# Optimization experiments

Hardware: AMD Instinct MI355X
Metric: run time of the kernel (lower is better)

## Reference

```python
import jax, jax.numpy as jnp
import numpy as np

HEADS = 4
DIM_HEAD = 128


def setup_inputs() -> dict:
    key = jax.random.key(0)
    k1, k2, k3 = jax.random.split(key, 3)
    dim = 256
    hidden = HEADS * DIM_HEAD  # 512
    x = jax.random.normal(k1, (16, dim, 64, 64), dtype=jnp.float32)
    # 1x1 conv weights stored as [out_ch, in_ch] (kernel dims squeezed)
    w_qkv = jax.random.normal(k2, (hidden * 3, dim), dtype=jnp.float32) * (1.0 / np.sqrt(dim))
    w_out = jax.random.normal(k3, (dim, hidden), dtype=jnp.float32) * (1.0 / np.sqrt(hidden))
    b_out = jnp.zeros((dim,), dtype=jnp.float32)
    return {"x": x, "w_qkv": w_qkv, "w_out": w_out, "b_out": b_out}


def reference(x, w_qkv, w_out, b_out):
    b, c, h, w = x.shape
    n = h * w
    # 1x1 conv == per-pixel linear projection
    qkv = jnp.einsum('bchw,oc->bohw', x, w_qkv)           # [b, 3*heads*dh, h, w]
    qkv = qkv.reshape(b, 3, HEADS, DIM_HEAD, n)           # 'b (qkv heads c) h w -> qkv b heads c (h w)'
    q, k, v = qkv[:, 0], qkv[:, 1], qkv[:, 2]             # [b, heads, dh, n]
    k = jax.nn.softmax(k, axis=-1)                        # softmax over spatial positions
    context = jnp.einsum('bhdn,bhen->bhde', k, v)         # [b, heads, dh, dh]
    out = jnp.einsum('bhde,bhdn->bhen', context, q)       # [b, heads, dh, n]
    out = out.reshape(b, HEADS * DIM_HEAD, h, w)          # 'b heads c (h w) -> b (heads c) h w'
    y = jnp.einsum('bchw,oc->bohw', out, w_out) + b_out[None, :, None, None]
    return y
```

## Files before the change

kernel.cpp:

```cpp
#include <hip/hip_runtime.h>

#define BATCH 16
#define CIN   256
#define NSP   4096
#define HID   512

typedef short v8s __attribute__((ext_vector_type(8)));
typedef float v4f __attribute__((ext_vector_type(4)));

__device__ __forceinline__ unsigned short f2bf(float f) {
    union { float f; unsigned u; } a; a.f = f;
    unsigned r = a.u + 0x7fffu + ((a.u >> 16) & 1u);
    return (unsigned short)(r >> 16);
}
__device__ __forceinline__ float bf2f(unsigned short s) {
    union { unsigned u; float f; } a; a.u = ((unsigned)s) << 16;
    return a.f;
}

__device__ __forceinline__ void gld_lds16(const unsigned short* g, unsigned short* l) {
    __builtin_amdgcn_global_load_lds(
        (const __attribute__((address_space(1))) unsigned int*)g,
        (__attribute__((address_space(3))) unsigned int*)l,
        16, 0, 0);
}

__global__ __launch_bounds__(256) void k_cvt_w(const float* __restrict__ wq,
                                               unsigned short* __restrict__ wbf) {
    const int t = blockIdx.x * 256 + threadIdx.x;
    const float4 f0 = *(const float4*)(wq + (size_t)t * 8);
    const float4 f1 = *(const float4*)(wq + (size_t)t * 8 + 4);
    union { unsigned short s[8]; uint4 u; } p;
    p.s[0] = f2bf(f0.x); p.s[1] = f2bf(f0.y); p.s[2] = f2bf(f0.z); p.s[3] = f2bf(f0.w);
    p.s[4] = f2bf(f1.x); p.s[5] = f2bf(f1.y); p.s[6] = f2bf(f1.z); p.s[7] = f2bf(f1.w);
    *(uint4*)(wbf + (size_t)t * 8) = p.u;
}

__global__ __launch_bounds__(256) void k_tr_wq(const float* __restrict__ wq,
                                               unsigned short* __restrict__ wqT) {
    __shared__ float tile[64 * 65];
    const int t = threadIdx.x;
    const int u0 = blockIdx.x * 64, c0 = blockIdx.y * 64;
    {
        const int cl = (t & 15) * 4, ul = t >> 4;
        #pragma unroll
        for (int i = 0; i < 4; i++) {
            int u = ul + i * 16;
            const float4 f = *(const float4*)(wq + (size_t)(u0 + u) * CIN + c0 + cl);
            *(float4*)(&tile[u * 65 + cl]) = f;
        }
    }
    __syncthreads();
    {
        const int ul4 = (t & 15) * 4, cl = t >> 4;
        #pragma unroll
        for (int i = 0; i < 4; i++) {
            int c = cl + i * 16;
            union { unsigned short s[4]; uint2 u; } p;
            #pragma unroll
            for (int j = 0; j < 4; j++)
                p.s[j] = f2bf(tile[(ul4 + j) * 65 + c]);
            *(uint2*)(wqT + (size_t)(c0 + c) * HID + u0 + ul4) = p.u;
        }
    }
}

__global__ __launch_bounds__(256) void k_prep(const float* __restrict__ x,
                                              unsigned short* __restrict__ xbf,
                                              unsigned short* __restrict__ xT) {
    __shared__ float tile[64 * 65];
    const int t = threadIdx.x;
    const int n0 = blockIdx.x * 64, c0 = blockIdx.y * 64, bz = blockIdx.z;
    const float* xb = x + (size_t)bz * CIN * NSP;
    {
        const int nl = (t & 15) * 4, cl = t >> 4;
        #pragma unroll
        for (int i = 0; i < 4; i++) {
            int c = cl + i * 16;
            const float4 f = *(const float4*)(xb + (size_t)(c0 + c) * NSP + n0 + nl);
            *(float4*)(&tile[c * 65 + nl]) = f;
            union { unsigned short s[4]; uint2 u; } p;
            p.s[0] = f2bf(f.x); p.s[1] = f2bf(f.y); p.s[2] = f2bf(f.z); p.s[3] = f2bf(f.w);
            *(uint2*)(xbf + ((size_t)bz * CIN + c0 + c) * NSP + n0 + nl) = p.u;
        }
    }
    __syncthreads();
    {
        const int cl4 = (t & 15) * 4, nl = t >> 4;
        #pragma unroll
        for (int i = 0; i < 4; i++) {
            int n = nl + i * 16;
            union { unsigned short s[4]; uint2 u; } p;
            #pragma unroll
            for (int j = 0; j < 4; j++)
                p.s[j] = f2bf(tile[(cl4 + j) * 65 + n]);
            *(uint2*)(xT + ((size_t)bz * NSP + n0 + n) * CIN + c0 + cl4) = p.u;
        }
    }
}

__global__ __launch_bounds__(256) void k_k(const unsigned short* __restrict__ wbf,
                                           const unsigned short* __restrict__ xT,
                                           unsigned short* __restrict__ expk,
                                           float* __restrict__ zp) {
    __shared__ __align__(16) unsigned short As[128 * 32];
    __shared__ __align__(16) unsigned short Bs[128 * 32];
    const int t = threadIdx.x;
    const int id = blockIdx.x;
    const int bz = id >> 7;
    const int r  = id & 127;
    const int xcd = r & 7, s = r >> 3;
    const int bn = (xcd << 2) | (s & 3);
    const int bm = s >> 2;
    const int m0 = bm * 128, n0 = bn * 128;
    const int lane = t & 63, wv = t >> 6;
    const int quad = lane >> 4, l15 = lane & 15;
    const int wm = (wv & 1) * 64, wn = (wv >> 1) * 64;

    const int srow = lane >> 2, scol = (lane & 3) * 8;
    unsigned short* Al0 = As + wv * 16 * 32;
    unsigned short* Al1 = Al0 + 64 * 32;
    unsigned short* Bl0 = Bs + wv * 16 * 32;
    unsigned short* Bl1 = Bl0 + 64 * 32;
    const unsigned short* Ag0 = wbf + (size_t)(512 + m0 + wv * 16 + srow) * CIN + scol;
    const unsigned short* Ag1 = Ag0 + 64 * CIN;
    const unsigned short* Bg0 = xT + ((size_t)bz * NSP + n0 + wv * 16 + srow) * CIN + scol;
    const unsigned short* Bg1 = Bg0 + 64 * CIN;

    v4f acc[4][4];
    #pragma unroll
    for (int i = 0; i < 4; i++)
        #pragma unroll
        for (int j = 0; j < 4; j++) acc[i][j] = (v4f)0.f;

    for (int kk = 0; kk < CIN; kk += 32) {
        gld_lds16(Ag0 + kk, Al0);
        gld_lds16(Ag1 + kk, Al1);
        gld_lds16(Bg0 + kk, Bl0);
        gld_lds16(Bg1 + kk, Bl1);
        __syncthreads();
        v8s af[4], bfr[4];
        #pragma unroll
        for (int mi = 0; mi < 4; mi++) {
            union { v8s v; uint4 u; } rr;
            rr.u = *(const uint4*)(&As[(wm + mi * 16 + l15) * 32 + quad * 8]);
            af[mi] = rr.v;
        }
        #pragma unroll
        for (int ni = 0; ni < 4; ni++) {
            union { v8s v; uint4 u; } rr;
            rr.u = *(const uint4*)(&Bs[(wn + ni * 16 + l15) * 32 + quad * 8]);
            bfr[ni] = rr.v;
        }
        #pragma unroll
        for (int mi = 0; mi < 4; mi++)
            #pragma unroll
            for (int ni = 0; ni < 4; ni++)
                acc[mi][ni] = __builtin_amdgcn_mfma_f32_16x16x32_bf16(af[mi], bfr[ni], acc[mi][ni], 0, 0, 0);
        __syncthreads();
    }

    float zr[4][4];
    #pragma unroll
    for (int mi = 0; mi < 4; mi++)
        #pragma unroll
        for (int rr = 0; rr < 4; rr++) zr[mi][rr] = 0.f;
    #pragma unroll
    for (int mi = 0; mi < 4; mi++)
        #pragma unroll
        for (int ni = 0; ni < 4; ni++)
            #pragma unroll
            for (int rr = 0; rr < 4; rr++) {
                float e = __expf(acc[mi][ni][rr]);
                acc[mi][ni][rr] = e;
                zr[mi][rr] += e;
            }
    #pragma unroll
    for (int mi = 0; mi < 4; mi++) {
        int row = m0 + wm + mi * 16 + quad * 4;
        #pragma unroll
        for (int ni = 0; ni < 4; ni++) {
            int n = n0 + wn + ni * 16 + l15;
            #pragma unroll
            for (int rr = 0; rr < 4; rr++)
                expk[((size_t)bz * 512 + row + rr) * NSP + n] = f2bf(acc[mi][ni][rr]);
        }
    }
    const int half = wv >> 1;
    #pragma unroll
    for (int mi = 0; mi < 4; mi++)
        #pragma unroll
        for (int rr = 0; rr < 4; rr++) {
            float z = zr[mi][rr];
            z += __shfl_xor(z, 1); z += __shfl_xor(z, 2);
            z += __shfl_xor(z, 4); z += __shfl_xor(z, 8);
            if (l15 == 0)
                zp[((size_t)bz * 512 + m0 + wm + mi * 16 + quad * 4 + rr) * 64 + bn * 2 + half] = z;
        }
}

__global__ __launch_bounds__(256) void k_S(const unsigned short* __restrict__ expk,
                                           const unsigned short* __restrict__ xbf,
                                           float* __restrict__ Sp) {
    __shared__ __align__(16) unsigned short As[128 * 32];
    __shared__ __align__(16) unsigned short Bs[128 * 32];
    const int t = threadIdx.x;
    const int id = blockIdx.x;
    const int hc = id >> 6;
    const int h = hc >> 1, ch = hc & 1;
    const int bkc = id & 63;
    const int b = bkc >> 2, kc = bkc & 3;
    const int kw = kc * 1024;
    const int lane = t & 63, wv = t >> 6, quad = lane >> 4, l15 = lane & 15;
    const int wm = (wv & 1) * 64, wn = (wv >> 1) * 64;

    const int srow = lane >> 2, scol = (lane & 3) * 8;
    unsigned short* Al0 = As + wv * 16 * 32;
    unsigned short* Al1 = Al0 + 64 * 32;
    unsigned short* Bl0 = Bs + wv * 16 * 32;
    unsigned short* Bl1 = Bl0 + 64 * 32;
    const unsigned short* Ag0 = expk + ((size_t)b * 512 + h * 128 + wv * 16 + srow) * NSP + kw + scol;
    const unsigned short* Ag1 = Ag0 + 64 * NSP;
    const unsigned short* Bg0 = xbf + ((size_t)b * CIN + ch * 128 + wv * 16 + srow) * NSP + kw + scol;
    const unsigned short* Bg1 = Bg0 + 64 * NSP;

    v4f acc[4][4];
    #pragma unroll
    for (int i = 0; i < 4; i++)
        #pragma unroll
        for (int j = 0; j < 4; j++) acc[i][j] = (v4f)0.f;

    for (int kk = 0; kk < 1024; kk += 32) {
        gld_lds16(Ag0 + kk, Al0);
        gld_lds16(Ag1 + kk, Al1);
        gld_lds16(Bg0 + kk, Bl0);
        gld_lds16(Bg1 + kk, Bl1);
        __syncthreads();
        v8s af[4], bfr[4];
        #pragma unroll
        for (int mi = 0; mi < 4; mi++) {
            union { v8s v; uint4 u; } rr;
            rr.u = *(const uint4*)(&As[(wm + mi * 16 + l15) * 32 + quad * 8]);
            af[mi] = rr.v;
        }
        #pragma unroll
        for (int ni = 0; ni < 4; ni++) {
            union { v8s v; uint4 u; } rr;
            rr.u = *(const uint4*)(&Bs[(wn + ni * 16 + l15) * 32 + quad * 8]);
            bfr[ni] = rr.v;
        }
        #pragma unroll
        for (int mi = 0; mi < 4; mi++)
            #pragma unroll
            for (int ni = 0; ni < 4; ni++)
                acc[mi][ni] = __builtin_amdgcn_mfma_f32_16x16x32_bf16(af[mi], bfr[ni], acc[mi][ni], 0, 0, 0);
        __syncthreads();
    }

    const int bh = b * 4 + h;
    float* outp = Sp + ((size_t)(bh * 2 + ch) * 4 + kc) * 16384;
    #pragma unroll
    for (int mi = 0; mi < 4; mi++)
        #pragma unroll
        for (int ni = 0; ni < 4; ni++)
            #pragma unroll
            for (int rr = 0; rr < 4; rr++)
                outp[(wm + mi * 16 + quad * 4 + rr) * 128 + wn + ni * 16 + l15] = acc[mi][ni][rr];
}

__global__ __launch_bounds__(256) void k_sred(const float* __restrict__ Sp,
                                              unsigned short* __restrict__ Sred) {
    const int qv = blockIdx.x * 256 + threadIdx.x;
    const int bh = qv >> 13, r = qv & 8191;
    const int dl = r >> 6, cq6 = r & 63;
    const int ch = cq6 >> 5, clq = cq6 & 31;
    const float* p = Sp + ((size_t)(bh * 2 + ch) * 4) * 16384 + dl * 128 + clq * 4;
    float4 s = *(const float4*)p;
    #pragma unroll
    for (int kc = 1; kc < 4; kc++) {
        const float4 f = *(const float4*)(p + (size_t)kc * 16384);
        s.x += f.x; s.y += f.y; s.z += f.z; s.w += f.w;
    }
    union { unsigned short us[4]; uint2 u; } pk;
    pk.us[0] = f2bf(s.x); pk.us[1] = f2bf(s.y); pk.us[2] = f2bf(s.z); pk.us[3] = f2bf(s.w);
    *(uint2*)(Sred + (size_t)bh * 32768 + dl * 256 + cq6 * 4) = pk.u;
}

__global__ __launch_bounds__(256) void k_redwc(const unsigned short* __restrict__ Sred,
                                               const float* __restrict__ zp,
                                               const unsigned short* __restrict__ wbf,
                                               const float* __restrict__ w_out,
                                               unsigned short* __restrict__ Wc) {
    __shared__ unsigned short Ds[128 * 136];
    __shared__ float zinv[128];
    const int t = threadIdx.x;
    const int bh = blockIdx.x;  const int b = bh >> 2, h = bh & 3;
    const int lane = t & 63, wv = t >> 6, quad = lane >> 4, l15 = lane & 15;

    if (t < 128) {
        float z = 0.f;
        #pragma unroll
        for (int nt = 0; nt < 64; nt++)
            z += zp[((size_t)b * 512 + h * 128 + t) * 64 + nt];
        zinv[t] = 1.0f / z;
    }
    __syncthreads();

    {
        const int wm = (wv & 1) * 64, wn = (wv >> 1) * 64;
        const unsigned short* Sb = Sred + (size_t)bh * 32768;
        const unsigned short* Vb = wbf + (size_t)(1024 + h * 128) * CIN;
        v4f acc[4][4];
        #pragma unroll
        for (int i = 0; i < 4; i++)
            #pragma unroll
            for (int j = 0; j < 4; j++) acc[i][j] = (v4f)0.f;
        for (int kk = 0; kk < CIN; kk += 32) {
            v8s af[4], bfr[4];
            #pragma unroll
            for (int mi = 0; mi < 4; mi++) {
                union { v8s v; uint4 u; } rr;
                rr.u = *(const uint4*)(Sb + (size_t)(wm + mi * 16 + l15) * 256 + kk + quad * 8);
                af[mi] = rr.v;
            }
            #pragma unroll
            for (int ni = 0; ni < 4; ni++) {
                union { v8s v; uint4 u; } rr;
                rr.u = *(const uint4*)(Vb + (size_t)(wn + ni * 16 + l15) * 256 + kk + quad * 8);
                bfr[ni] = rr.v;
            }
            #pragma unroll
            for (int mi = 0; mi < 4; mi++)
                #pragma unroll
                for (int ni = 0; ni < 4; ni++)
                    acc[mi][ni] = __builtin_amdgcn_mfma_f32_16x16x32_bf16(af[mi], bfr[ni], acc[mi][ni], 0, 0, 0);
        }
        float zq[4][4];
        #pragma unroll
        for (int mi = 0; mi < 4; mi++)
            #pragma unroll
            for (int rr = 0; rr < 4; rr++)
                zq[mi][rr] = zinv[wm + mi * 16 + quad * 4 + rr];
        #pragma unroll
        for (int mi = 0; mi < 4; mi++)
            #pragma unroll
            for (int ni = 0; ni < 4; ni++)
                #pragma unroll
                for (int rr = 0; rr < 4; rr++)
                    Ds[(wm + mi * 16 + quad * 4 + rr) * 136 + wn + ni * 16 + l15] =
                        f2bf(acc[mi][ni][rr] * zq[mi][rr]);
    }
    __syncthreads();

    {
        const int wm = wv * 64;
        v4f acc[4][8];
        #pragma unroll
        for (int i = 0; i < 4; i++)
            #pragma unroll
            for (int j = 0; j < 8; j++) acc[i][j] = (v4f)0.f;
        for (int kk = 0; kk < 128; kk += 32) {
            v8s af[4], bfr[8];
            #pragma unroll
            for (int mi = 0; mi < 4; mi++) {
                int o = wm + mi * 16 + l15;
                const float* wp = w_out + (size_t)o * HID + h * 128 + kk + quad * 8;
                float4 f0 = *(const float4*)wp;
                float4 f1 = *(const float4*)(wp + 4);
                union { v8s v; unsigned short s[8]; } r;
                r.s[0] = f2bf(f0.x); r.s[1] = f2bf(f0.y); r.s[2] = f2bf(f0.z); r.s[3] = f2bf(f0.w);
                r.s[4] = f2bf(f1.x); r.s[5] = f2bf(f1.y); r.s[6] = f2bf(f1.z); r.s[7] = f2bf(f1.w);
                af[mi] = r.v;
            }
            #pragma unroll
            for (int ni = 0; ni < 8; ni++) {
                const unsigned short* p = &Ds[(ni * 16 + l15) * 136 + kk + quad * 8];
                union { v8s v; uint4 u; } r;
                r.u = *(const uint4*)p;
                bfr[ni] = r.v;
            }
            #pragma unroll
            for (int mi = 0; mi < 4; mi++)
                #pragma unroll
                for (int ni = 0; ni < 8; ni++)
                    acc[mi][ni] = __builtin_amdgcn_mfma_f32_16x16x32_bf16(af[mi], bfr[ni], acc[mi][ni], 0, 0, 0);
        }
        #pragma unroll
        for (int ni = 0; ni < 8; ni++) {
            int d = ni * 16 + l15;
            #pragma unroll
            for (int mi = 0; mi < 4; mi++)
                #pragma unroll
                for (int rr = 0; rr < 4; rr++) {
                    int o = wm + mi * 16 + quad * 4 + rr;
                    Wc[((size_t)b * 256 + o) * HID + h * 128 + d] = f2bf(acc[mi][ni][rr]);
                }
        }
    }
}

__global__ __launch_bounds__(256) void k_chain(const unsigned short* __restrict__ Wc,
                                               const unsigned short* __restrict__ wqT,
                                               unsigned short* __restrict__ Weff) {
    __shared__ __align__(16) unsigned short As[128 * 32];
    __shared__ __align__(16) unsigned short Bs[128 * 32];
    const int t = threadIdx.x;
    const int m0 = blockIdx.x * 128, n0 = blockIdx.y * 128, bz = blockIdx.z;
    const int lane = t & 63, wv = t >> 6, quad = lane >> 4, l15 = lane & 15;
    const int wm = (wv & 1) * 64, wn = (wv >> 1) * 64;

    const int srow = lane >> 2, scol = (lane & 3) * 8;
    unsigned short* Al0 = As + wv * 16 * 32;
    unsigned short* Al1 = Al0 + 64 * 32;
    unsigned short* Bl0 = Bs + wv * 16 * 32;
    unsigned short* Bl1 = Bl0 + 64 * 32;
    const unsigned short* Ag0 = Wc + ((size_t)bz * 256 + m0 + wv * 16 + srow) * HID + scol;
    const unsigned short* Ag1 = Ag0 + 64 * HID;
    const unsigned short* Bg0 = wqT + (size_t)(n0 + wv * 16 + srow) * HID + scol;
    const unsigned short* Bg1 = Bg0 + 64 * HID;

    v4f acc[4][4];
    #pragma unroll
    for (int i = 0; i < 4; i++)
        #pragma unroll
        for (int j = 0; j < 4; j++) acc[i][j] = (v4f)0.f;

    for (int kk = 0; kk < HID; kk += 32) {
        gld_lds16(Ag0 + kk, Al0);
        gld_lds16(Ag1 + kk, Al1);
        gld_lds16(Bg0 + kk, Bl0);
        gld_lds16(Bg1 + kk, Bl1);
        __syncthreads();
        v8s af[4], bfr[4];
        #pragma unroll
        for (int mi = 0; mi < 4; mi++) {
            union { v8s v; uint4 u; } rr;
            rr.u = *(const uint4*)(&As[(wm + mi * 16 + l15) * 32 + quad * 8]);
            af[mi] = rr.v;
        }
        #pragma unroll
        for (int ni = 0; ni < 4; ni++) {
            union { v8s v; uint4 u; } rr;
            rr.u = *(const uint4*)(&Bs[(wn + ni * 16 + l15) * 32 + quad * 8]);
            bfr[ni] = rr.v;
        }
        #pragma unroll
        for (int mi = 0; mi < 4; mi++)
            #pragma unroll
            for (int ni = 0; ni < 4; ni++)
                acc[mi][ni] = __builtin_amdgcn_mfma_f32_16x16x32_bf16(af[mi], bfr[ni], acc[mi][ni], 0, 0, 0);
        __syncthreads();
    }
    #pragma unroll
    for (int mi = 0; mi < 4; mi++) {
        int obase = m0 + wm + mi * 16 + quad * 4;
        #pragma unroll
        for (int ni = 0; ni < 4; ni++) {
            int c = n0 + wn + ni * 16 + l15;
            #pragma unroll
            for (int r = 0; r < 4; r++)
                Weff[((size_t)bz * 256 + obase + r) * 256 + c] = f2bf(acc[mi][ni][r]);
        }
    }
}

__global__ __launch_bounds__(256) void k_y(const unsigned short* __restrict__ Weff,
                                           const unsigned short* __restrict__ xT,
                                           const float* __restrict__ b_out,
                                           float* __restrict__ y) {
    __shared__ __align__(16) unsigned short As[128 * 32];
    __shared__ __align__(16) unsigned short Bs[128 * 32];
    const int t = threadIdx.x;
    const int m0 = blockIdx.x * 128;
    const int n0 = blockIdx.y * 128;
    const int bz = blockIdx.z;
    const int lane = t & 63, wv = t >> 6, quad = lane >> 4, l15 = lane & 15;
    const int wm = (wv & 1) * 64, wn = (wv >> 1) * 64;

    const int srow = lane >> 2, scol = (lane & 3) * 8;
    unsigned short* Al0 = As + wv * 16 * 32;
    unsigned short* Al1 = Al0 + 64 * 32;
    unsigned short* Bl0 = Bs + wv * 16 * 32;
    unsigned short* Bl1 = Bl0 + 64 * 32;
    const unsigned short* Ag0 = Weff + ((size_t)bz * 256 + m0 + wv * 16 + srow) * CIN + scol;
    const unsigned short* Ag1 = Ag0 + 64 * CIN;
    const unsigned short* Bg0 = xT + ((size_t)bz * NSP + n0 + wv * 16 + srow) * CIN + scol;
    const unsigned short* Bg1 = Bg0 + 64 * CIN;

    v4f acc[4][4];
    #pragma unroll
    for (int i = 0; i < 4; i++)
        #pragma unroll
        for (int j = 0; j < 4; j++) acc[i][j] = (v4f)0.f;

    for (int kk = 0; kk < CIN; kk += 32) {
        gld_lds16(Ag0 + kk, Al0);
        gld_lds16(Ag1 + kk, Al1);
        gld_lds16(Bg0 + kk, Bl0);
        gld_lds16(Bg1 + kk, Bl1);
        __syncthreads();
        v8s af[4], bfr[4];
        #pragma unroll
        for (int mi = 0; mi < 4; mi++) {
            union { v8s v; uint4 u; } rr;
            rr.u = *(const uint4*)(&As[(wm + mi * 16 + l15) * 32 + quad * 8]);
            af[mi] = rr.v;
        }
        #pragma unroll
        for (int ni = 0; ni < 4; ni++) {
            union { v8s v; uint4 u; } rr;
            rr.u = *(const uint4*)(&Bs[(wn + ni * 16 + l15) * 32 + quad * 8]);
            bfr[ni] = rr.v;
        }
        #pragma unroll
        for (int mi = 0; mi < 4; mi++)
            #pragma unroll
            for (int ni = 0; ni < 4; ni++)
                acc[mi][ni] = __builtin_amdgcn_mfma_f32_16x16x32_bf16(af[mi], bfr[ni], acc[mi][ni], 0, 0, 0);
        __syncthreads();
    }
    #pragma unroll
    for (int mi = 0; mi < 4; mi++) {
        int o = m0 + wm + mi * 16 + quad * 4;
        #pragma unroll
        for (int ni = 0; ni < 4; ni++) {
            int n = n0 + wn + ni * 16 + l15;
            #pragma unroll
            for (int r = 0; r < 4; r++)
                y[((size_t)bz * 256 + o + r) * NSP + n] = acc[mi][ni][r] + b_out[o + r];
        }
    }
}

extern "C" void kernel_launch(void* const* d_in, const int* in_sizes, int n_in,
                              void* d_out, int out_size, void* d_ws, size_t ws_size,
                              hipStream_t stream) {
    (void)in_sizes; (void)n_in; (void)out_size; (void)ws_size;
    const float* x     = (const float*)d_in[0];
    const float* w_qkv = (const float*)d_in[1];
    const float* w_out = (const float*)d_in[2];
    const float* b_out = (const float*)d_in[3];
    float* y = (float*)d_out;
    char* ws = (char*)d_ws;

    unsigned short* xT   = (unsigned short*)(ws);
    unsigned short* xbf  = (unsigned short*)(ws + 33554432);
    unsigned short* expk = (unsigned short*)(ws + 67108864);
    float*          Sp   = (float*)(ws + 134217728);
    float*          zp   = (float*)(ws + 167772160);
    unsigned short* Sred = (unsigned short*)(ws + 176160768);
    unsigned short* Wc   = (unsigned short*)(ws + 180355072);
    unsigned short* Weff = (unsigned short*)(ws + 184549376);
    unsigned short* wbf  = (unsigned short*)(ws + 186646528);
    unsigned short* wqT  = (unsigned short*)(ws + 187432960);

    k_cvt_w<<<dim3(192),        256, 0, stream>>>(w_qkv, wbf);
    k_tr_wq<<<dim3(8, 4),       256, 0, stream>>>(w_qkv, wqT);
    k_prep <<<dim3(64, 4, 16),  256, 0, stream>>>(x, xbf, xT);
    k_k    <<<dim3(2048),       256, 0, stream>>>(wbf, xT, expk, zp);
    k_S    <<<dim3(512),        256, 0, stream>>>(expk, xbf, Sp);
    k_sred <<<dim3(2048),       256, 0, stream>>>(Sp, Sred);
    k_redwc<<<dim3(64),         256, 0, stream>>>(Sred, zp, wbf, w_out, Wc);
    k_chain<<<dim3(2, 2, 16),   256, 0, stream>>>(Wc, wqT, Weff);
    k_y    <<<dim3(2, 32, 16),  256, 0, stream>>>(Weff, xT, b_out, y);
}
```

Before: 262.2 us.

## Swap GEMM operand roles for vectorized epilogue stores and merge weight prep kernels

Swaps the A/B operands in the k_k, k_S, k_chain and k_y GEMMs so that each thread's four accumulator rows are contiguous along the output's fastest dimension. Epilogue stores become 8- or 16-byte vector writes instead of scalar 2- or 4-byte strided writes. The exp-sum reduction in k_k is redone to match the new fragment mapping. It also merges the two weight-preparation kernels into one launch to save a kernel launch. Store coalescing per instruction changes: lanes now spread across rows rather than along one row.

```diff
diff --git a/kernel.cpp b/kernel.cpp
--- a/kernel.cpp
+++ b/kernel.cpp
@@ -25,22 +25,24 @@
         16, 0, 0);
 }
 
-__global__ __launch_bounds__(256) void k_cvt_w(const float* __restrict__ wq,
-                                               unsigned short* __restrict__ wbf) {
-    const int t = blockIdx.x * 256 + threadIdx.x;
-    const float4 f0 = *(const float4*)(wq + (size_t)t * 8);
-    const float4 f1 = *(const float4*)(wq + (size_t)t * 8 + 4);
-    union { unsigned short s[8]; uint4 u; } p;
-    p.s[0] = f2bf(f0.x); p.s[1] = f2bf(f0.y); p.s[2] = f2bf(f0.z); p.s[3] = f2bf(f0.w);
-    p.s[4] = f2bf(f1.x); p.s[5] = f2bf(f1.y); p.s[6] = f2bf(f1.z); p.s[7] = f2bf(f1.w);
-    *(uint4*)(wbf + (size_t)t * 8) = p.u;
-}
-
-__global__ __launch_bounds__(256) void k_tr_wq(const float* __restrict__ wq,
-                                               unsigned short* __restrict__ wqT) {
+__global__ __launch_bounds__(256) void k_w(const float* __restrict__ wq,
+                                           unsigned short* __restrict__ wbf,
+                                           unsigned short* __restrict__ wqT) {
+    const int bid = blockIdx.x;
+    if (bid < 192) {
+        const int t = bid * 256 + threadIdx.x;
+        const float4 f0 = *(const float4*)(wq + (size_t)t * 8);
+        const float4 f1 = *(const float4*)(wq + (size_t)t * 8 + 4);
+        union { unsigned short s[8]; uint4 u; } p;
+        p.s[0] = f2bf(f0.x); p.s[1] = f2bf(f0.y); p.s[2] = f2bf(f0.z); p.s[3] = f2bf(f0.w);
+        p.s[4] = f2bf(f1.x); p.s[5] = f2bf(f1.y); p.s[6] = f2bf(f1.z); p.s[7] = f2bf(f1.w);
+        *(uint4*)(wbf + (size_t)t * 8) = p.u;
+        return;
+    }
     __shared__ float tile[64 * 65];
-    const int t = threadIdx.x;
-    const int u0 = blockIdx.x * 64, c0 = blockIdx.y * 64;
+    const int bb = bid - 192;
+    const int u0 = (bb & 7) * 64, c0 = (bb >> 3) * 64;
+    const int t = threadIdx.x;
     {
         const int cl = (t & 15) * 4, ul = t >> 4;
         #pragma unroll
@@ -112,19 +114,19 @@
     const int xcd = r & 7, s = r >> 3;
     const int bn = (xcd << 2) | (s & 3);
     const int bm = s >> 2;
-    const int m0 = bm * 128, n0 = bn * 128;
+    const int d0 = bm * 128, n0 = bn * 128;
     const int lane = t & 63, wv = t >> 6;
     const int quad = lane >> 4, l15 = lane & 15;
-    const int wm = (wv & 1) * 64, wn = (wv >> 1) * 64;
+    const int wmN = (wv & 1) * 64, wnD = (wv >> 1) * 64;
 
     const int srow = lane >> 2, scol = (lane & 3) * 8;
     unsigned short* Al0 = As + wv * 16 * 32;
     unsigned short* Al1 = Al0 + 64 * 32;
     unsigned short* Bl0 = Bs + wv * 16 * 32;
     unsigned short* Bl1 = Bl0 + 64 * 32;
-    const unsigned short* Ag0 = wbf + (size_t)(512 + m0 + wv * 16 + srow) * CIN + scol;
+    const unsigned short* Ag0 = xT + ((size_t)bz * NSP + n0 + wv * 16 + srow) * CIN + scol;
     const unsigned short* Ag1 = Ag0 + 64 * CIN;
-    const unsigned short* Bg0 = xT + ((size_t)bz * NSP + n0 + wv * 16 + srow) * CIN + scol;
+    const unsigned short* Bg0 = wbf + (size_t)(512 + d0 + wv * 16 + srow) * CIN + scol;
     const unsigned short* Bg1 = Bg0 + 64 * CIN;
 
     v4f acc[4][4];
@@ -143,13 +145,13 @@
         #pragma unroll
         for (int mi = 0; mi < 4; mi++) {
             union { v8s v; uint4 u; } rr;
-            rr.u = *(const uint4*)(&As[(wm + mi * 16 + l15) * 32 + quad * 8]);
+            rr.u = *(const uint4*)(&As[(wmN + mi * 16 + l15) * 32 + quad * 8]);
             af[mi] = rr.v;
         }
         #pragma unroll
         for (int ni = 0; ni < 4; ni++) {
             union { v8s v; uint4 u; } rr;
-            rr.u = *(const uint4*)(&Bs[(wn + ni * 16 + l15) * 32 + quad * 8]);
+            rr.u = *(const uint4*)(&Bs[(wnD + ni * 16 + l15) * 32 + quad * 8]);
             bfr[ni] = rr.v;
         }
         #pragma unroll
@@ -160,43 +162,31 @@
         __syncthreads();
     }
 
-    float zr[4][4];
-    #pragma unroll
-    for (int mi = 0; mi < 4; mi++)
-        #pragma unroll
-        for (int rr = 0; rr < 4; rr++) zr[mi][rr] = 0.f;
-    #pragma unroll
-    for (int mi = 0; mi < 4; mi++)
-        #pragma unroll
-        for (int ni = 0; ni < 4; ni++)
+    float zacc[4] = {0.f, 0.f, 0.f, 0.f};
+    #pragma unroll
+    for (int ni = 0; ni < 4; ni++) {
+        const int d = d0 + wnD + ni * 16 + l15;
+        #pragma unroll
+        for (int mi = 0; mi < 4; mi++) {
+            const int nb = n0 + wmN + mi * 16 + quad * 4;
+            union { unsigned short s[4]; uint2 u; } p;
             #pragma unroll
             for (int rr = 0; rr < 4; rr++) {
                 float e = __expf(acc[mi][ni][rr]);
-                acc[mi][ni][rr] = e;
-                zr[mi][rr] += e;
+                zacc[ni] += e;
+                p.s[rr] = f2bf(e);
             }
-    #pragma unroll
-    for (int mi = 0; mi < 4; mi++) {
-        int row = m0 + wm + mi * 16 + quad * 4;
-        #pragma unroll
-        for (int ni = 0; ni < 4; ni++) {
-            int n = n0 + wn + ni * 16 + l15;
-            #pragma unroll
-            for (int rr = 0; rr < 4; rr++)
-                expk[((size_t)bz * 512 + row + rr) * NSP + n] = f2bf(acc[mi][ni][rr]);
-        }
-    }
-    const int half = wv >> 1;
-    #pragma unroll
-    for (int mi = 0; mi < 4; mi++)
-        #pragma unroll
-        for (int rr = 0; rr < 4; rr++) {
-            float z = zr[mi][rr];
-            z += __shfl_xor(z, 1); z += __shfl_xor(z, 2);
-            z += __shfl_xor(z, 4); z += __shfl_xor(z, 8);
-            if (l15 == 0)
-                zp[((size_t)bz * 512 + m0 + wm + mi * 16 + quad * 4 + rr) * 64 + bn * 2 + half] = z;
-        }
+            *(uint2*)(expk + ((size_t)bz * 512 + d) * NSP + nb) = p.u;
+        }
+    }
+    #pragma unroll
+    for (int ni = 0; ni < 4; ni++) {
+        float z = zacc[ni];
+        z += __shfl_xor(z, 16);
+        z += __shfl_xor(z, 32);
+        if (quad == 0)
+            zp[((size_t)bz * 512 + d0 + wnD + ni * 16 + l15) * 64 + bn * 2 + (wv & 1)] = z;
+    }
 }
 
 __global__ __launch_bounds__(256) void k_S(const unsigned short* __restrict__ expk,
@@ -212,16 +202,16 @@
     const int b = bkc >> 2, kc = bkc & 3;
     const int kw = kc * 1024;
     const int lane = t & 63, wv = t >> 6, quad = lane >> 4, l15 = lane & 15;
-    const int wm = (wv & 1) * 64, wn = (wv >> 1) * 64;
+    const int wmC = (wv & 1) * 64, wnD = (wv >> 1) * 64;
 
     const int srow = lane >> 2, scol = (lane & 3) * 8;
     unsigned short* Al0 = As + wv * 16 * 32;
     unsigned short* Al1 = Al0 + 64 * 32;
     unsigned short* Bl0 = Bs + wv * 16 * 32;
     unsigned short* Bl1 = Bl0 + 64 * 32;
-    const unsigned short* Ag0 = expk + ((size_t)b * 512 + h * 128 + wv * 16 + srow) * NSP + kw + scol;
+    const unsigned short* Ag0 = xbf + ((size_t)b * CIN + ch * 128 + wv * 16 + srow) * NSP + kw + scol;
     const unsigned short* Ag1 = Ag0 + 64 * NSP;
-    const unsigned short* Bg0 = xbf + ((size_t)b * CIN + ch * 128 + wv * 16 + srow) * NSP + kw + scol;
+    const unsigned short* Bg0 = expk + ((size_t)b * 512 + h * 128 + wv * 16 + srow) * NSP + kw + scol;
     const unsigned short* Bg1 = Bg0 + 64 * NSP;
 
     v4f acc[4][4];
@@ -240,13 +230,13 @@
         #pragma unroll
         for (int mi = 0; mi < 4; mi++) {
             union { v8s v; uint4 u; } rr;
-            rr.u = *(const uint4*)(&As[(wm + mi * 16 + l15) * 32 + quad * 8]);
+            rr.u = *(const uint4*)(&As[(wmC + mi * 16 + l15) * 32 + quad * 8]);
             af[mi] = rr.v;
         }
         #pragma unroll
         for (int ni = 0; ni < 4; ni++) {
             union { v8s v; uint4 u; } rr;
-            rr.u = *(const uint4*)(&Bs[(wn + ni * 16 + l15) * 32 + quad * 8]);
+            rr.u = *(const uint4*)(&Bs[(wnD + ni * 16 + l15) * 32 + quad * 8]);
             bfr[ni] = rr.v;
         }
         #pragma unroll
@@ -260,12 +250,14 @@
     const int bh = b * 4 + h;
     float* outp = Sp + ((size_t)(bh * 2 + ch) * 4 + kc) * 16384;
     #pragma unroll
-    for (int mi = 0; mi < 4; mi++)
-        #pragma unroll
-        for (int ni = 0; ni < 4; ni++)
-            #pragma unroll
-            for (int rr = 0; rr < 4; rr++)
-                outp[(wm + mi * 16 + quad * 4 + rr) * 128 + wn + ni * 16 + l15] = acc[mi][ni][rr];
+    for (int ni = 0; ni < 4; ni++) {
+        const int d = wnD + ni * 16 + l15;
+        #pragma unroll
+        for (int mi = 0; mi < 4; mi++) {
+            const int c = wmC + mi * 16 + quad * 4;
+            *(v4f*)(outp + d * 128 + c) = acc[mi][ni];
+        }
+    }
 }
 
 __global__ __launch_bounds__(256) void k_sred(const float* __restrict__ Sp,
@@ -405,18 +397,18 @@
     __shared__ __align__(16) unsigned short As[128 * 32];
     __shared__ __align__(16) unsigned short Bs[128 * 32];
     const int t = threadIdx.x;
-    const int m0 = blockIdx.x * 128, n0 = blockIdx.y * 128, bz = blockIdx.z;
+    const int c0 = blockIdx.x * 128, o0 = blockIdx.y * 128, bz = blockIdx.z;
     const int lane = t & 63, wv = t >> 6, quad = lane >> 4, l15 = lane & 15;
-    const int wm = (wv & 1) * 64, wn = (wv >> 1) * 64;
+    const int wmC = (wv & 1) * 64, wnO = (wv >> 1) * 64;
 
     const int srow = lane >> 2, scol = (lane & 3) * 8;
     unsigned short* Al0 = As + wv * 16 * 32;
     unsigned short* Al1 = Al0 + 64 * 32;
     unsigned short* Bl0 = Bs + wv * 16 * 32;
     unsigned short* Bl1 = Bl0 + 64 * 32;
-    const unsigned short* Ag0 = Wc + ((size_t)bz * 256 + m0 + wv * 16 + srow) * HID + scol;
+    const unsigned short* Ag0 = wqT + (size_t)(c0 + wv * 16 + srow) * HID + scol;
     const unsigned short* Ag1 = Ag0 + 64 * HID;
-    const unsigned short* Bg0 = wqT + (size_t)(n0 + wv * 16 + srow) * HID + scol;
+    const unsigned short* Bg0 = Wc + ((size_t)bz * 256 + o0 + wv * 16 + srow) * HID + scol;
     const unsigned short* Bg1 = Bg0 + 64 * HID;
 
     v4f acc[4][4];
@@ -435,13 +427,13 @@
         #pragma unroll
         for (int mi = 0; mi < 4; mi++) {
             union { v8s v; uint4 u; } rr;
-            rr.u = *(const uint4*)(&As[(wm + mi * 16 + l15) * 32 + quad * 8]);
+            rr.u = *(const uint4*)(&As[(wmC + mi * 16 + l15) * 32 + quad * 8]);
             af[mi] = rr.v;
         }
         #pragma unroll
         for (int ni = 0; ni < 4; ni++) {
             union { v8s v; uint4 u; } rr;
-            rr.u = *(const uint4*)(&Bs[(wn + ni * 16 + l15) * 32 + quad * 8]);
+            rr.u = *(const uint4*)(&Bs[(wnO + ni * 16 + l15) * 32 + quad * 8]);
             bfr[ni] = rr.v;
         }
         #pragma unroll
@@ -452,14 +444,15 @@
         __syncthreads();
     }
     #pragma unroll
-    for (int mi = 0; mi < 4; mi++) {
-        int obase = m0 + wm + mi * 16 + quad * 4;
-        #pragma unroll
-        for (int ni = 0; ni < 4; ni++) {
-            int c = n0 + wn + ni * 16 + l15;
-            #pragma unroll
-            for (int r = 0; r < 4; r++)
-                Weff[((size_t)bz * 256 + obase + r) * 256 + c] = f2bf(acc[mi][ni][r]);
+    for (int ni = 0; ni < 4; ni++) {
+        const int o = o0 + wnO + ni * 16 + l15;
+        #pragma unroll
+        for (int mi = 0; mi < 4; mi++) {
+            const int c = c0 + wmC + mi * 16 + quad * 4;
+            union { unsigned short s[4]; uint2 u; } p;
+            #pragma unroll
+            for (int rr = 0; rr < 4; rr++) p.s[rr] = f2bf(acc[mi][ni][rr]);
+            *(uint2*)(Weff + ((size_t)bz * 256 + o) * 256 + c) = p.u;
         }
     }
 }
@@ -471,20 +464,20 @@
     __shared__ __align__(16) unsigned short As[128 * 32];
     __shared__ __align__(16) unsigned short Bs[128 * 32];
     const int t = threadIdx.x;
-    const int m0 = blockIdx.x * 128;
+    const int o0 = blockIdx.x * 128;
     const int n0 = blockIdx.y * 128;
     const int bz = blockIdx.z;
     const int lane = t & 63, wv = t >> 6, quad = lane >> 4, l15 = lane & 15;
-    const int wm = (wv & 1) * 64, wn = (wv >> 1) * 64;
+    const int wmN = (wv & 1) * 64, wnO = (wv >> 1) * 64;
 
     const int srow = lane >> 2, scol = (lane & 3) * 8;
     unsigned short* Al0 = As + wv * 16 * 32;
     unsigned short* Al1 = Al0 + 64 * 32;
     unsigned short* Bl0 = Bs + wv * 16 * 32;
     unsigned short* Bl1 = Bl0 + 64 * 32;
-    const unsigned short* Ag0 = Weff + ((size_t)bz * 256 + m0 + wv * 16 + srow) * CIN + scol;
+    const unsigned short* Ag0 = xT + ((size_t)bz * NSP + n0 + wv * 16 + srow) * CIN + scol;
     const unsigned short* Ag1 = Ag0 + 64 * CIN;
-    const unsigned short* Bg0 = xT + ((size_t)bz * NSP + n0 + wv * 16 + srow) * CIN + scol;
+    const unsigned short* Bg0 = Weff + ((size_t)bz * 256 + o0 + wv * 16 + srow) * CIN + scol;
     const unsigned short* Bg1 = Bg0 + 64 * CIN;
 
     v4f acc[4][4];
@@ -503,13 +496,13 @@
         #pragma unroll
         for (int mi = 0; mi < 4; mi++) {
             union { v8s v; uint4 u; } rr;
-            rr.u = *(const uint4*)(&As[(wm + mi * 16 + l15) * 32 + quad * 8]);
+            rr.u = *(const uint4*)(&As[(wmN + mi * 16 + l15) * 32 + quad * 8]);
             af[mi] = rr.v;
         }
         #pragma unroll
         for (int ni = 0; ni < 4; ni++) {
             union { v8s v; uint4 u; } rr;
-            rr.u = *(const uint4*)(&Bs[(wn + ni * 16 + l15) * 32 + quad * 8]);
+            rr.u = *(const uint4*)(&Bs[(wnO + ni * 16 + l15) * 32 + quad * 8]);
             bfr[ni] = rr.v;
         }
         #pragma unroll
@@ -520,14 +513,15 @@
         __syncthreads();
     }
     #pragma unroll
-    for (int mi = 0; mi < 4; mi++) {
-        int o = m0 + wm + mi * 16 + quad * 4;
-        #pragma unroll
-        for (int ni = 0; ni < 4; ni++) {
-            int n = n0 + wn + ni * 16 + l15;
-            #pragma unroll
-            for (int r = 0; r < 4; r++)
-                y[((size_t)bz * 256 + o + r) * NSP + n] = acc[mi][ni][r] + b_out[o + r];
+    for (int ni = 0; ni < 4; ni++) {
+        const int o = o0 + wnO + ni * 16 + l15;
+        const float bias = b_out[o];
+        #pragma unroll
+        for (int mi = 0; mi < 4; mi++) {
+            const int n = n0 + wmN + mi * 16 + quad * 4;
+            v4f v = acc[mi][ni];
+            v[0] += bias; v[1] += bias; v[2] += bias; v[3] += bias;
+            *(v4f*)(y + ((size_t)bz * 256 + o) * NSP + n) = v;
         }
     }
 }
@@ -554,8 +548,7 @@
     unsigned short* wbf  = (unsigned short*)(ws + 186646528);
     unsigned short* wqT  = (unsigned short*)(ws + 187432960);
 
-    k_cvt_w<<<dim3(192),        256, 0, stream>>>(w_qkv, wbf);
-    k_tr_wq<<<dim3(8, 4),       256, 0, stream>>>(w_qkv, wqT);
+    k_w    <<<dim3(224),        256, 0, stream>>>(w_qkv, wbf, wqT);
     k_prep <<<dim3(64, 4, 16),  256, 0, stream>>>(x, xbf, xT);
     k_k    <<<dim3(2048),       256, 0, stream>>>(wbf, xT, expk, zp);
     k_S    <<<dim3(512),        256, 0, stream>>>(expk, xbf, Sp);
```

Result: no change. 259.6 us (-1.0%).
